# Kernel optimization log

Hardware: AMD Instinct MI355X
Metric: run time of the kernel (lower is better)

## Reference

```python
import jax, jax.numpy as jnp
import numpy as np

TEMPERATURE = 0.07
BASE_TEMPERATURE = 0.07
L_MAX = 16  # max number of session labels per dialogue
NEG_INF = -1e30


def setup_inputs() -> dict:
    key = jax.random.key(0)
    k1, k2, k3 = jax.random.split(key, 3)
    B, T, H = 128, 1024, 256
    features = jax.random.normal(k1, (B, T, H), dtype=jnp.float32)
    dialogue_lengths = jax.random.randint(k2, (B,), 1, T + 1)
    labels = jax.random.randint(k3, (B, T), 0, L_MAX)
    return {"features": features, "dialogue_lengths": dialogue_lengths, "labels": labels}


def reference(features, dialogue_lengths, labels):
    B, T, H = features.shape
    valid = jnp.arange(T)[None, :] < dialogue_lengths[:, None]            # [B,T]
    # one-hot label assignment, zeroed at padded positions
    oh = (labels[..., None] == jnp.arange(L_MAX)[None, None, :]) & valid[..., None]
    ohf = oh.astype(features.dtype)                                       # [B,T,L]
    counts = ohf.sum(axis=1)                                              # [B,L]
    # per-dialogue, per-label prototype = mean of member features
    proto_sum = jnp.einsum('btl,bth->blh', ohf, features)                 # [B,L,H]
    prototypes = proto_sum / jnp.maximum(counts, 1.0)[..., None]          # [B,L,H]
    # anchor-vs-prototype logits
    logits = jnp.einsum('bth,blh->btl', features, prototypes) / TEMPERATURE
    present = counts > 0                                                  # [B,L]
    logits = jnp.where(present[:, None, :], logits, NEG_INF)
    log_prob = jax.nn.log_softmax(logits, axis=-1)                        # [B,T,L]
    # mask is one-hot on each token's own label -> mean_log_prob_pos is log_prob at own label
    pos = jnp.take_along_axis(log_prob, labels[..., None], axis=-1)[..., 0]  # [B,T]
    tok_loss = -(TEMPERATURE / BASE_TEMPERATURE) * pos
    per_dialogue = jnp.sum(jnp.where(valid, tok_loss, 0.0), axis=1) / dialogue_lengths.astype(features.dtype)
    return per_dialogue.mean()
```

## Files before the change

### kernel.cpp

```cpp
#include <hip/hip_runtime.h>
#include <math.h>

#define B 128
#define T 1024
#define H 256
#define L 16
#define INV_TEMP (1.0f/0.07f)
#define NEG_INF -1e30f


__global__ __launch_bounds__(256) void proto_kernel(
    const float* __restrict__ feat, const int* __restrict__ dlen,
    const int* __restrict__ labels, float* __restrict__ ws_pp,
    int* __restrict__ ws_cntp, float* __restrict__ out) {
  __shared__ float acc[4][L * 128];
  __shared__ int labs[256];
  __shared__ int cnt[L];

  const int bx = blockIdx.x;
  if (bx == 0 && threadIdx.x == 0) out[0] = 0.f;

  const int b = bx >> 3;
  const int chunk = (bx >> 2) & 1;
  const int seg = bx & 3;
  const int tid = threadIdx.x;
  const int w = tid >> 6;
  const int lane = tid & 63;

  const int len = dlen[b];
  if (seg * 256 >= len) return;

  for (int i = tid; i < 4 * L * 128 / 4; i += 256)
    ((float4*)acc)[i] = make_float4(0.f, 0.f, 0.f, 0.f);
  labs[tid] = labels[(size_t)b * T + seg * 256 + tid];
  if (tid < L) cnt[tid] = 0;
  __syncthreads();

  if (chunk == 0 && (seg * 256 + tid) < len) atomicAdd(&cnt[labs[tid]], 1);

  int nt = len - seg * 256 - w * 64;
  if (nt > 64) nt = 64;
  const float2* fbase = (const float2*)(feat +
      ((size_t)b * T + seg * 256 + w * 64) * H + chunk * 128);
  float* a = acc[w];

  int j = 0;
  for (; j + 4 <= nt; j += 4) {
    float2 f0 = fbase[(size_t)(j + 0) * (H / 2) + lane];
    float2 f1 = fbase[(size_t)(j + 1) * (H / 2) + lane];
    float2 f2 = fbase[(size_t)(j + 2) * (H / 2) + lane];
    float2 f3 = fbase[(size_t)(j + 3) * (H / 2) + lane];
    const int l0 = labs[w * 64 + j + 0];
    const int l1 = labs[w * 64 + j + 1];
    const int l2 = labs[w * 64 + j + 2];
    const int l3 = labs[w * 64 + j + 3];
    float2* p0 = (float2*)&a[l0 * 128 + lane * 2];
    { float2 v = *p0; v.x += f0.x; v.y += f0.y; *p0 = v; }
    float2* p1 = (float2*)&a[l1 * 128 + lane * 2];
    { float2 v = *p1; v.x += f1.x; v.y += f1.y; *p1 = v; }
    float2* p2 = (float2*)&a[l2 * 128 + lane * 2];
    { float2 v = *p2; v.x += f2.x; v.y += f2.y; *p2 = v; }
    float2* p3 = (float2*)&a[l3 * 128 + lane * 2];
    { float2 v = *p3; v.x += f3.x; v.y += f3.y; *p3 = v; }
  }
  for (; j < nt; ++j) {
    float2 f = fbase[(size_t)j * (H / 2) + lane];
    const int lab = labs[w * 64 + j];
    float2* p = (float2*)&a[lab * 128 + lane * 2];
    float2 v = *p; v.x += f.x; v.y += f.y; *p = v;
  }
  __syncthreads();

  float* op = ws_pp + (((size_t)b * 4 + seg) * L) * H + chunk * 128;
  for (int e = tid; e < L * 128 / 4; e += 256) {
    const float4 s0 = ((const float4*)acc[0])[e];
    const float4 s1 = ((const float4*)acc[1])[e];
    const float4 s2 = ((const float4*)acc[2])[e];
    const float4 s3 = ((const float4*)acc[3])[e];
    float4 s;
    s.x = s0.x + s1.x + s2.x + s3.x;
    s.y = s0.y + s1.y + s2.y + s3.y;
    s.z = s0.z + s1.z + s2.z + s3.z;
    s.w = s0.w + s1.w + s2.w + s3.w;
    *(float4*)&op[(e >> 5) * H + ((e & 31) << 2)] = s;
  }
  if (chunk == 0 && tid < L) ws_cntp[(b * 4 + seg) * L + tid] = cnt[tid];
}

#define DOT_BODY(CB, FR)                                                   \
  _Pragma("unroll") for (int q = 0; q < 4; ++q) {                          \
    _Pragma("unroll") for (int l = 0; l < L; ++l) {                        \
      const float4 p = *(const float4*)&pr[l * H + (CB) * 16 + q * 4];     \
      dot[l] += FR[q].x * p.x + FR[q].y * p.y +                            \
                FR[q].z * p.z + FR[q].w * p.w;                             \
    }                                                                      \
  }

__global__ __launch_bounds__(128, 4) void dotsloss_kernel(
    const float* __restrict__ feat, const int* __restrict__ dlen,
    const int* __restrict__ labels, const float* __restrict__ ws_pp,
    const int* __restrict__ ws_cntp, float* __restrict__ out) {
  __shared__ float pr[L * H];
  __shared__ int cnts[L];
  __shared__ float red[128];

  const int b = blockIdx.x >> 3;
  const int oct = blockIdx.x & 7;
  const int tid = threadIdx.x;

  const int len = dlen[b];
  if (oct * 128 >= len) return;
  const int nseg = (len + 255) >> 8;

  if (tid < L) {
    const int* cp = ws_cntp + b * 4 * L + tid;
    int c = 0;
    for (int s = 0; s < nseg; ++s) c += cp[s * L];
    cnts[tid] = c;
  }
  __syncthreads();

  const float4* gp4 = (const float4*)(ws_pp + (size_t)b * 4 * L * H);
  for (int i = tid; i < L * H / 4; i += 128) {
    const int l = i >> 6;
    float4 s = gp4[i];
    for (int sg = 1; sg < nseg; ++sg) {
      const float4 t2 = gp4[sg * (L * 64) + i];
      s.x += t2.x; s.y += t2.y; s.z += t2.z; s.w += t2.w;
    }
    const int cn = cnts[l];
    const float inv = (cn > 0) ? 1.f / (float)cn : 0.f;
    ((float4*)pr)[i] = make_float4(s.x * inv, s.y * inv, s.z * inv, s.w * inv);
  }
  __syncthreads();

  const int t = oct * 128 + tid;
  float tok = 0.f;

  if (t < len) {
    const float4* f4 = (const float4*)(feat + ((size_t)b * T + t) * H);
    float dot[L];
#pragma unroll
    for (int l = 0; l < L; ++l) dot[l] = 0.f;

    float4 fa[4], fb[4];
#pragma unroll
    for (int q = 0; q < 4; ++q) fa[q] = f4[q];

    for (int cb = 0; cb < 14; cb += 2) {
#pragma unroll
      for (int q = 0; q < 4; ++q) fb[q] = f4[(cb + 1) * 4 + q];
      DOT_BODY(cb, fa);
#pragma unroll
      for (int q = 0; q < 4; ++q) fa[q] = f4[(cb + 2) * 4 + q];
      DOT_BODY(cb + 1, fb);
    }
#pragma unroll
    for (int q = 0; q < 4; ++q) fb[q] = f4[15 * 4 + q];
    DOT_BODY(14, fa);
    DOT_BODY(15, fb);

    float lg[L];
#pragma unroll
    for (int l = 0; l < L; ++l)
      lg[l] = (cnts[l] > 0) ? dot[l] * INV_TEMP : NEG_INF;
    float m = lg[0];
#pragma unroll
    for (int l = 1; l < L; ++l) m = fmaxf(m, lg[l]);
    float se = 0.f;
#pragma unroll
    for (int l = 0; l < L; ++l) se += expf(lg[l] - m);
    const float lsp = m + logf(se);

    const int lab = labels[(size_t)b * T + t];
    float pos = 0.f;
#pragma unroll
    for (int l = 0; l < L; ++l) pos += (l == lab) ? lg[l] : 0.f;

    tok = lsp - pos;
  }

  red[tid] = tok;
  __syncthreads();
#pragma unroll
  for (int s = 64; s > 0; s >>= 1) {
    if (tid < s) red[tid] += red[tid + s];
    __syncthreads();
  }
  if (tid == 0) atomicAdd(out, red[0] / ((float)len * (float)B));
}

extern "C" void kernel_launch(void* const* d_in, const int* in_sizes, int n_in,
                              void* d_out, int out_size, void* d_ws, size_t ws_size,
                              hipStream_t stream) {
  const float* feat = (const float*)d_in[0];
  const int* dlen = (const int*)d_in[1];
  const int* labels = (const int*)d_in[2];
  float* out = (float*)d_out;

  float* ws_pp = (float*)d_ws;
  int* ws_cntp = (int*)(ws_pp + (size_t)B * 4 * L * H);

  proto_kernel<<<B * 8, 256, 0, stream>>>(feat, dlen, labels, ws_pp,
                                          ws_cntp, out);
  dotsloss_kernel<<<B * 8, 128, 0, stream>>>(feat, dlen, labels, ws_pp,
                                             ws_cntp, out);
}
```

Baseline: 239.7 us.

## Use shared-memory atomics with float4 loads and component-split accumulator in proto kernel

The proto kernel drops the per-wave private accumulators. All waves now share one accumulator laid out as [component][label][32], updated with shared-memory atomicAdd. Each lane loads a float4 and half-waves handle alternating tokens. This shrinks LDS use from 32KB to 8KB and widens global loads, at the price of LDS atomic contention when tokens in a wave share a label and extra atomic instruction overhead.

```diff
diff --git a/kernel.cpp b/kernel.cpp
--- a/kernel.cpp
+++ b/kernel.cpp
@@ -13,7 +13,7 @@
     const float* __restrict__ feat, const int* __restrict__ dlen,
     const int* __restrict__ labels, float* __restrict__ ws_pp,
     int* __restrict__ ws_cntp, float* __restrict__ out) {
-  __shared__ float acc[4][L * 128];
+  __shared__ float acc[4][L][32];
   __shared__ int labs[256];
   __shared__ int cnt[L];
 
@@ -24,13 +24,11 @@
   const int chunk = (bx >> 2) & 1;
   const int seg = bx & 3;
   const int tid = threadIdx.x;
-  const int w = tid >> 6;
-  const int lane = tid & 63;
 
   const int len = dlen[b];
   if (seg * 256 >= len) return;
 
-  for (int i = tid; i < 4 * L * 128 / 4; i += 256)
+  for (int i = tid; i < 4 * L * 32 / 4; i += 256)
     ((float4*)acc)[i] = make_float4(0.f, 0.f, 0.f, 0.f);
   labs[tid] = labels[(size_t)b * T + seg * 256 + tid];
   if (tid < L) cnt[tid] = 0;
@@ -38,51 +36,53 @@
 
   if (chunk == 0 && (seg * 256 + tid) < len) atomicAdd(&cnt[labs[tid]], 1);
 
+  const int w = tid >> 6;
+  const int lane = tid & 63;
+  const int half = lane >> 5;
+  const int m = lane & 31;
+
   int nt = len - seg * 256 - w * 64;
   if (nt > 64) nt = 64;
-  const float2* fbase = (const float2*)(feat +
+  const float4* fb = (const float4*)(feat +
       ((size_t)b * T + seg * 256 + w * 64) * H + chunk * 128);
-  float* a = acc[w];
-
-  int j = 0;
-  for (; j + 4 <= nt; j += 4) {
-    float2 f0 = fbase[(size_t)(j + 0) * (H / 2) + lane];
-    float2 f1 = fbase[(size_t)(j + 1) * (H / 2) + lane];
-    float2 f2 = fbase[(size_t)(j + 2) * (H / 2) + lane];
-    float2 f3 = fbase[(size_t)(j + 3) * (H / 2) + lane];
-    const int l0 = labs[w * 64 + j + 0];
-    const int l1 = labs[w * 64 + j + 1];
-    const int l2 = labs[w * 64 + j + 2];
-    const int l3 = labs[w * 64 + j + 3];
-    float2* p0 = (float2*)&a[l0 * 128 + lane * 2];
-    { float2 v = *p0; v.x += f0.x; v.y += f0.y; *p0 = v; }
-    float2* p1 = (float2*)&a[l1 * 128 + lane * 2];
-    { float2 v = *p1; v.x += f1.x; v.y += f1.y; *p1 = v; }
-    float2* p2 = (float2*)&a[l2 * 128 + lane * 2];
-    { float2 v = *p2; v.x += f2.x; v.y += f2.y; *p2 = v; }
-    float2* p3 = (float2*)&a[l3 * 128 + lane * 2];
-    { float2 v = *p3; v.x += f3.x; v.y += f3.y; *p3 = v; }
-  }
-  for (; j < nt; ++j) {
-    float2 f = fbase[(size_t)j * (H / 2) + lane];
-    const int lab = labs[w * 64 + j];
-    float2* p = (float2*)&a[lab * 128 + lane * 2];
-    float2 v = *p; v.x += f.x; v.y += f.y; *p = v;
+
+  if (nt == 64) {
+    for (int j = 0; j < 32; j += 4) {
+      const float4 f0 = fb[(size_t)(2 * j + 0 + half) * 64 + m];
+      const float4 f1 = fb[(size_t)(2 * j + 2 + half) * 64 + m];
+      const float4 f2 = fb[(size_t)(2 * j + 4 + half) * 64 + m];
+      const float4 f3 = fb[(size_t)(2 * j + 6 + half) * 64 + m];
+      const int l0 = labs[w * 64 + 2 * j + 0 + half];
+      const int l1 = labs[w * 64 + 2 * j + 2 + half];
+      const int l2 = labs[w * 64 + 2 * j + 4 + half];
+      const int l3 = labs[w * 64 + 2 * j + 6 + half];
+      atomicAdd(&acc[0][l0][m], f0.x); atomicAdd(&acc[1][l0][m], f0.y);
+      atomicAdd(&acc[2][l0][m], f0.z); atomicAdd(&acc[3][l0][m], f0.w);
+      atomicAdd(&acc[0][l1][m], f1.x); atomicAdd(&acc[1][l1][m], f1.y);
+      atomicAdd(&acc[2][l1][m], f1.z); atomicAdd(&acc[3][l1][m], f1.w);
+      atomicAdd(&acc[0][l2][m], f2.x); atomicAdd(&acc[1][l2][m], f2.y);
+      atomicAdd(&acc[2][l2][m], f2.z); atomicAdd(&acc[3][l2][m], f2.w);
+      atomicAdd(&acc[0][l3][m], f3.x); atomicAdd(&acc[1][l3][m], f3.y);
+      atomicAdd(&acc[2][l3][m], f3.z); atomicAdd(&acc[3][l3][m], f3.w);
+    }
+  } else {
+    for (int j = 0; j < 32; ++j) {
+      const int tr = 2 * j + half;
+      if (tr >= nt) break;
+      const float4 f = fb[(size_t)tr * 64 + m];
+      const int l = labs[w * 64 + tr];
+      atomicAdd(&acc[0][l][m], f.x); atomicAdd(&acc[1][l][m], f.y);
+      atomicAdd(&acc[2][l][m], f.z); atomicAdd(&acc[3][l][m], f.w);
+    }
   }
   __syncthreads();
 
   float* op = ws_pp + (((size_t)b * 4 + seg) * L) * H + chunk * 128;
-  for (int e = tid; e < L * 128 / 4; e += 256) {
-    const float4 s0 = ((const float4*)acc[0])[e];
-    const float4 s1 = ((const float4*)acc[1])[e];
-    const float4 s2 = ((const float4*)acc[2])[e];
-    const float4 s3 = ((const float4*)acc[3])[e];
-    float4 s;
-    s.x = s0.x + s1.x + s2.x + s3.x;
-    s.y = s0.y + s1.y + s2.y + s3.y;
-    s.z = s0.z + s1.z + s2.z + s3.z;
-    s.w = s0.w + s1.w + s2.w + s3.w;
-    *(float4*)&op[(e >> 5) * H + ((e & 31) << 2)] = s;
+  for (int e = tid; e < L * 32; e += 256) {
+    const int l = e >> 5, mm = e & 31;
+    const float4 s = make_float4(acc[0][l][mm], acc[1][l][mm],
+                                 acc[2][l][mm], acc[3][l][mm]);
+    *(float4*)&op[l * H + mm * 4] = s;
   }
   if (chunk == 0 && tid < L) ws_cntp[(b * 4 + seg) * L + tid] = cnt[tid];
 }
```

After: 377.3 us. 57.4% more time.
